# Kernel tuning notes

Hardware: AMD Instinct MI355X
Metric: run time of the kernel (lower is better)

Reference implementation:

```python
import jax, jax.numpy as jnp
import numpy as np

N, E, D_IN, HID, HEADS, TS_OUT = 100000, 200000, 165, 64, 8, 5
HD1 = HID // HEADS  # 8 per-head channels in layer 1
HD2 = HID           # 64 per-head channels in layer 2 (concat=False -> mean)


def _glorot(key, shape):
    fan_in, fan_out = shape[0], shape[1]
    s = np.sqrt(6.0 / (fan_in + fan_out)).astype(np.float32)
    return jax.random.uniform(key, shape, jnp.float32, -s, s)


def setup_inputs() -> dict:
    key = jax.random.key(0)
    ks = jax.random.split(key, 24)
    inp = {
        "x": jax.random.normal(ks[0], (N, D_IN), jnp.float32),
        "edge_index": jax.random.randint(ks[1], (2, E), 0, N, jnp.int32),
        "timestamp_target": jax.random.randint(ks[2], (N,), 0, TS_OUT, jnp.int32),
        "node_target": jax.random.randint(ks[3], (N,), 0, 2, jnp.int32),
        "node_mask": jax.random.randint(ks[4], (N,), 0, 2, jnp.int32).astype(jnp.bool_),
        # GATConv layer 1: in=165 -> 8 heads x 8 ch, concat -> 64
        "W1": _glorot(ks[5], (D_IN, HEADS * HD1)),
        "att_src1": _glorot(ks[6], (HEADS, HD1)),
        "att_dst1": _glorot(ks[7], (HEADS, HD1)),
        "b1": jnp.zeros((HEADS * HD1,), jnp.float32),
        # GATConv layer 2: in=64 -> 8 heads x 64 ch, mean -> 64
        "W2": _glorot(ks[8], (HID, HEADS * HD2)),
        "att_src2": _glorot(ks[9], (HEADS, HD2)),
        "att_dst2": _glorot(ks[10], (HEADS, HD2)),
        "b2": jnp.zeros((HD2,), jnp.float32),
        # timestamp predictor MLP
        "ts_w1": _glorot(ks[11], (HID, HID)), "ts_b1": jnp.zeros((HID,), jnp.float32),
        "ts_w2": _glorot(ks[12], (HID, TS_OUT)), "ts_b2": jnp.zeros((TS_OUT,), jnp.float32),
        # class predictor MLP
        "cls_w1": _glorot(ks[13], (HID, HID)), "cls_b1": jnp.zeros((HID,), jnp.float32),
        "cls_w2": _glorot(ks[14], (HID, 2)), "cls_b2": jnp.zeros((2,), jnp.float32),
    }
    return inp


def _gat_layer(x, src, dst, n, W, a_src, a_dst, b, concat):
    H, C = a_src.shape
    h = (x @ W).reshape(n, H, C)                      # [N,H,C]
    a_s = (h * a_src).sum(-1)                         # [N,H]
    a_d = (h * a_dst).sum(-1)                         # [N,H]
    alpha = jax.nn.leaky_relu(a_s[src] + a_d[dst], 0.2)   # [E,H]
    amax = jax.ops.segment_max(alpha, dst, num_segments=n)
    ea = jnp.exp(alpha - amax[dst])
    denom = jax.ops.segment_sum(ea, dst, num_segments=n)
    a = ea / (denom[dst] + 1e-16)                     # segment softmax over incoming edges
    out = jax.ops.segment_sum(h[src] * a[:, :, None], dst, num_segments=n)  # [N,H,C]
    out = out.reshape(n, H * C) if concat else out.mean(axis=1)
    return out + b


def _ce(logits, targets):
    lp = jax.nn.log_softmax(logits, axis=-1)
    return -jnp.take_along_axis(lp, targets[:, None].astype(jnp.int32), axis=1)[:, 0]


def reference(x, edge_index, timestamp_target, node_target, node_mask,
              W1, att_src1, att_dst1, b1, W2, att_src2, att_dst2, b2,
              ts_w1, ts_b1, ts_w2, ts_b2, cls_w1, cls_b1, cls_w2, cls_b2):
    n = x.shape[0]
    loops = jnp.arange(n, dtype=edge_index.dtype)
    src = jnp.concatenate([edge_index[0], loops])     # add self loops (PyG default)
    dst = jnp.concatenate([edge_index[1], loops])
    h = _gat_layer(x, src, dst, n, W1, att_src1, att_dst1, b1, True)   # [N,64]
    h = _gat_layer(h, src, dst, n, W2, att_src2, att_dst2, b2, False)  # [N,64]
    # gradient reversal is identity in the forward pass
    ts_pred = jax.nn.relu(h @ ts_w1 + ts_b1) @ ts_w2 + ts_b2           # [N,5]
    cls_pred = jax.nn.relu(h @ cls_w1 + cls_b1) @ cls_w2 + cls_b2      # [N,2]
    ts_loss = _ce(ts_pred, timestamp_target).mean()
    m = node_mask.astype(jnp.float32)
    cls_loss = (_ce(cls_pred, node_target) * m).sum() / m.sum()
    return cls_loss + 1.0 * ts_loss
```

## Files before the change

### kernel.cpp

```cpp
#include <hip/hip_runtime.h>
#include <hip/hip_bf16.h>

#define NN 100000
#define NE 200000
#define NT (NE + NN)
#define DIN 165
#define CHUNK 50000
#define PREPB 128
#define INITB 391
#define PACKB 8
#define W1PB 24
#define MISCGRID (PREPB + INITB + PACKB + W1PB)
#define NODEB 1563

typedef __attribute__((ext_vector_type(8))) short bf16x8_t;
typedef __attribute__((ext_vector_type(4))) float f32x4_t;
typedef _Float16 h2_t __attribute__((ext_vector_type(2)));
typedef _Float16 f16x8_t __attribute__((ext_vector_type(8)));

#define AS1 __attribute__((address_space(1)))
#define AS3 __attribute__((address_space(3)))

static __device__ __forceinline__ unsigned short f2bf(float f) {
    __hip_bfloat16 b = __float2bfloat16(f);
    return *(unsigned short*)&b;
}
static __device__ __forceinline__ float bfu(unsigned short u) {
    __hip_bfloat16 b = *(__hip_bfloat16*)&u;
    return __bfloat162float(b);
}
static __device__ __forceinline__ unsigned pkh2(float a, float b) {
    h2_t v; v[0] = (_Float16)a; v[1] = (_Float16)b;
    return *(unsigned*)&v;
}


__global__ __launch_bounds__(256) void k_misc(const float* W2, const float* a2s, const float* a2d,
                                              float* wsd, __hip_bfloat16* W2pT,
                                              int* cnt, int* fill,
                                              const float* tsw1, const float* cw1,
                                              unsigned* tswp, unsigned* cwp,
                                              const float* W1, unsigned* W1pT, float* zbuf) {
    int b = blockIdx.x;
    int tid = threadIdx.x;
    if (b < PREPB) {
        int i = b * 256 + tid;
        int c = i >> 9, j = i & 511;
        int hh = j >> 6, kk = j & 63;
        W2pT[i] = __float2bfloat16(W2[kk * 512 + hh * 64 + c]);
        if (b == 0 && tid < 64) zbuf[tid] = 0.f;
        if (i < 512) {
            int h = i >> 6, k = i & 63;
            float s = 0.f, d = 0.f;
            for (int cc = 0; cc < 64; cc++) {
                float w = W2[k * 512 + h * 64 + cc];
                s += w * a2s[h * 64 + cc];
                d += w * a2d[h * 64 + cc];
            }
            wsd[i] = s; wsd[512 + i] = d;
        }
    } else if (b < PREPB + INITB) {
        int i = (b - PREPB) * 256 + tid;
        if (i < NN) { cnt[i] = 0; fill[i] = 0; }
    } else if (b < PREPB + INITB + PACKB) {
        int i = (b - PREPB - INITB) * 256 + tid;
        if (i < 2048) {
            int kp = i >> 6, c = i & 63;
            tswp[i] = pkh2(tsw1[(2 * kp) * 64 + c], tsw1[(2 * kp + 1) * 64 + c]);
            cwp[i]  = pkh2(cw1[(2 * kp) * 64 + c],  cw1[(2 * kp + 1) * 64 + c]);
        }
    } else {
        int i = (b - PREPB - INITB - PACKB) * 256 + tid;
        if (i < 6144) {
            int c = i / 96, kp = i - c * 96;
            int k = 2 * kp;
            float f0 = (k < DIN) ? W1[k * 64 + c] : 0.f;
            float f1 = (k + 1 < DIN) ? W1[(k + 1) * 64 + c] : 0.f;
            W1pT[i] = pkh2(f0, f1);
        }
    }
}


__global__ __launch_bounds__(256) void k_count(const int* dstE, int* cnt) {
    int e = blockIdx.x * 256 + threadIdx.x;
    if (e < NE) atomicAdd(&cnt[dstE[e]], 1);
}

__global__ __launch_bounds__(256) void k_scanA(const int* cnt, int* rowptr, int* bsum) {
    __shared__ int sm[256];
    int t = threadIdx.x;
    int base = blockIdx.x * 1024;
    int v[4]; int s = 0;
    for (int i = 0; i < 4; i++) {
        int idx = base + t * 4 + i;
        v[i] = (idx < NN) ? (cnt[idx] + 1) : 0;
        s += v[i];
    }
    sm[t] = s; __syncthreads();
    for (int off = 1; off < 256; off <<= 1) {
        int x = (t >= off) ? sm[t - off] : 0;
        __syncthreads();
        sm[t] += x;
        __syncthreads();
    }
    int run = sm[t] - s;
    for (int i = 0; i < 4; i++) {
        run += v[i];
        int idx = base + t * 4 + i;
        if (idx < NN) rowptr[idx + 1] = run;
    }
    if (t == 255) bsum[blockIdx.x] = sm[255];
}

__global__ __launch_bounds__(64) void k_scanB(int* bsum, int nb) {
    int lane = threadIdx.x;
    int v0 = (lane < nb) ? bsum[lane] : 0;
    int v1 = (64 + lane < nb) ? bsum[64 + lane] : 0;
    int s0 = v0;
    for (int off = 1; off < 64; off <<= 1) { int t = __shfl_up(s0, off); if (lane >= off) s0 += t; }
    int tot0 = __shfl(s0, 63);
    int s1 = v1;
    for (int off = 1; off < 64; off <<= 1) { int t = __shfl_up(s1, off); if (lane >= off) s1 += t; }
    if (lane < nb) bsum[lane] = s0 - v0;
    if (64 + lane < nb) bsum[64 + lane] = tot0 + s1 - v1;
}

__global__ __launch_bounds__(256) void k_scanC(const int* bsum, int* rowptr) {
    int i = blockIdx.x * 256 + threadIdx.x;
    if (i < NN) rowptr[i + 1] += bsum[i >> 10];
    if (i == 0) rowptr[0] = 0;
}

__global__ __launch_bounds__(256) void k_fill(const int* srcE, const int* dstE,
                                              const int* rowptr, int* fill, int* col, int* rowv) {
    int i = blockIdx.x * 256 + threadIdx.x;
    if (i >= NT) return;
    int s, d;
    if (i < NE) { s = srcE[i]; d = dstE[i]; }
    else        { s = i - NE; d = s; }
    int p = rowptr[d] + atomicAdd(&fill[d], 1);
    col[p] = s;
    rowv[p] = d;
}


__global__ __launch_bounds__(256) void k_gemm1(const float* x, const unsigned* W1pT,
                                               const float* att_s, const float* att_d,
                                               const float* zsrc,
                                               __hip_bfloat16* h1b, float* aad1) {
    __shared__ float As[4][3 * 512];
    int tid = threadIdx.x;
    int l = tid & 63, w = tid >> 6;
    int n0 = blockIdx.x * 64 + w * 16;
    float* bufs = As[w];
    int frow = l & 15;
    int kg = l >> 4;
    int rl = l >> 5;
    int j2 = l & 3;
    int pb = (l >> 2) & 7;
    f32x4_t acc[4] = {};

#define G1_DMA(S, BI)                                                              \
    {                                                                              \
        float* dst_ = bufs + (BI) * 512;                                           \
        _Pragma("unroll")                                                          \
        for (int i_ = 0; i_ < 8; i_++) {                                           \
            int r_ = i_ * 2 + rl;                                                  \
            int kk_ = ((pb ^ (r_ & 7)) << 2) | j2;                                 \
            int k_ = (S) * 32 + kk_;                                               \
            int n_ = n0 + r_;                                                      \
            const float* g_ = (n_ < NN && k_ < DIN) ? (x + (size_t)n_ * DIN + k_)  \
                                                    : (zsrc + l);                  \
            __builtin_amdgcn_global_load_lds((const AS1 float*)g_,                 \
                                             (AS3 float*)(dst_ + i_ * 64), 4, 0, 0); \
        }                                                                          \
    }

#define G1_LB(DST, S)                                                              \
    _Pragma("unroll")                                                              \
    for (int t_ = 0; t_ < 4; t_++)                                                 \
        DST[t_] = *(const uint4*)&W1pT[(t_ * 16 + frow) * 96 + (S) * 16 + kg * 4];

#define G1_STEP(S, VM)                                                             \
    {                                                                              \
        __builtin_amdgcn_sched_barrier(0);                                         \
        if ((S) < 5) { G1_LB(Bn, (S) + 1) }                                        \
        __builtin_amdgcn_sched_barrier(0);                                         \
        if ((S) < 4) { G1_DMA((S) + 2, ((S) + 2) % 3) }                            \
        __builtin_amdgcn_sched_barrier(0);                                         \
        asm volatile("s_waitcnt vmcnt(" #VM ")" ::: "memory");                     \
        __builtin_amdgcn_sched_barrier(0);                                         \
        {                                                                          \
            float* cb_ = bufs + ((S) % 3) * 512;                                   \
            int b0_ = ((2 * kg) ^ (frow & 7)) * 4;                                 \
            int b1_ = ((2 * kg + 1) ^ (frow & 7)) * 4;                             \
            float4 f0 = *(const float4*)&cb_[frow * 32 + b0_];                     \
            float4 f1 = *(const float4*)&cb_[frow * 32 + b1_];                     \
            f16x8_t av;                                                            \
            av[0] = (_Float16)f0.x; av[1] = (_Float16)f0.y;                        \
            av[2] = (_Float16)f0.z; av[3] = (_Float16)f0.w;                        \
            av[4] = (_Float16)f1.x; av[5] = (_Float16)f1.y;                        \
            av[6] = (_Float16)f1.z; av[7] = (_Float16)f1.w;                        \
            _Pragma("unroll")                                                      \
            for (int t_ = 0; t_ < 4; t_++)                                         \
                acc[t_] = __builtin_amdgcn_mfma_f32_16x16x32_f16(                  \
                    av, *(f16x8_t*)&Bn0[t_], acc[t_], 0, 0, 0);                    \
            _Pragma("unroll")                                                      \
            for (int t_ = 0; t_ < 4; t_++) Bn0[t_] = Bn[t_];                       \
        }                                                                          \
    }

    uint4 Bn0[4], Bn[4];
    G1_DMA(0, 0)
    G1_DMA(1, 1)
    G1_LB(Bn0, 0)
    G1_STEP(0, 12)
    G1_STEP(1, 20)
    G1_STEP(2, 20)
    G1_STEP(3, 20)
    G1_STEP(4, 12)
    G1_STEP(5, 0)

    unsigned short* h1u = (unsigned short*)h1b;
    float asv[4], adv[4];
    #pragma unroll
    for (int t = 0; t < 4; t++) {
        int c = t * 16 + frow;
        asv[t] = att_s[c]; adv[t] = att_d[c];
    }
    int hb = (l >> 3) & 1;
    #pragma unroll
    for (int q = 0; q < 4; q++) {
        int n = n0 + kg * 4 + q;
        bool ok = (n < NN);
        #pragma unroll
        for (int t = 0; t < 4; t++) {
            if (ok) h1u[(size_t)n * 64 + t * 16 + frow] = f2bf(acc[t][q]);
            float sv = acc[t][q] * asv[t];
            float dv = acc[t][q] * adv[t];
            sv += __shfl_xor(sv, 1); sv += __shfl_xor(sv, 2); sv += __shfl_xor(sv, 4);
            dv += __shfl_xor(dv, 1); dv += __shfl_xor(dv, 2); dv += __shfl_xor(dv, 4);
            if (ok && (l & 7) == 0) {
                int h = t * 2 + hb;
                aad1[(size_t)n * 16 + h]     = sv;
                aad1[(size_t)n * 16 + 8 + h] = dv;
            }
        }
    }
}


__global__ __launch_bounds__(256) void k_edgew(const float* aad, const int* col, const int* rowv,
                                               __hip_bfloat16* web) {
    int e = blockIdx.x * 256 + threadIdx.x;
    if (e >= NT) return;
    int s = col[e], d = rowv[e];
    float4 s0 = *(const float4*)&aad[(size_t)s * 16];
    float4 s1 = *(const float4*)&aad[(size_t)s * 16 + 4];
    float4 dd0 = *(const float4*)&aad[(size_t)d * 16 + 8];
    float4 dd1 = *(const float4*)&aad[(size_t)d * 16 + 12];
    float as[8] = {s0.x, s0.y, s0.z, s0.w, s1.x, s1.y, s1.z, s1.w};
    float ad[8] = {dd0.x, dd0.y, dd0.z, dd0.w, dd1.x, dd1.y, dd1.z, dd1.w};
    unsigned p[4];
    #pragma unroll
    for (int q = 0; q < 4; q++) {
        float a0 = as[2*q]   + ad[2*q];
        float a1 = as[2*q+1] + ad[2*q+1];
        a0 = a0 > 0.f ? a0 : 0.2f * a0;
        a1 = a1 > 0.f ? a1 : 0.2f * a1;
        p[q] = (unsigned)f2bf(__expf(a0)) | ((unsigned)f2bf(__expf(a1)) << 16);
    }
    *(uint4*)&web[(size_t)e * 8] = make_uint4(p[0], p[1], p[2], p[3]);
}


__global__ __launch_bounds__(256) void k_agg1(const __hip_bfloat16* h1b, const __hip_bfloat16* we1b,
                                              const int* rowptr, const int* col,
                                              const float* b1, __hip_bfloat16* out1b) {
    int tid = threadIdx.x;
    int q = tid & 15;
    int n = blockIdx.x * 16 + (tid >> 4);
    int hq = q >> 1;
    const unsigned short* h1u = (const unsigned short*)h1b;
    const unsigned short* weu = (const unsigned short*)we1b;
    int rs = rowptr[n], re = rowptr[n + 1];
    float acc0 = 0.f, acc1 = 0.f, acc2 = 0.f, acc3 = 0.f, den = 0.f;
    for (int eb = rs; eb < re; eb += 4) {
        int c4[4];
        #pragma unroll
        for (int j = 0; j < 4; j++) c4[j] = col[min(eb + j, re - 1)];
        #pragma unroll
        for (int j = 0; j < 4; j++) {
            int e = min(eb + j, re - 1);
            float wv = bfu(weu[(size_t)e * 8 + hq]);
            wv = (eb + j < re) ? wv : 0.f;
            uint2 hv = *(const uint2*)&h1u[(size_t)c4[j] * 64 + q * 4];
            den  += wv;
            acc0 += wv * bfu((unsigned short)(hv.x & 0xffff));
            acc1 += wv * bfu((unsigned short)(hv.x >> 16));
            acc2 += wv * bfu((unsigned short)(hv.y & 0xffff));
            acc3 += wv * bfu((unsigned short)(hv.y >> 16));
        }
    }
    float4 bb = *(const float4*)&b1[q * 4];
    float dd = den + 1e-16f;
    unsigned short* ou = (unsigned short*)out1b;
    unsigned p0 = (unsigned)f2bf(acc0 / dd + bb.x) | ((unsigned)f2bf(acc1 / dd + bb.y) << 16);
    unsigned p1 = (unsigned)f2bf(acc2 / dd + bb.z) | ((unsigned)f2bf(acc3 / dd + bb.w) << 16);
    *(uint2*)&ou[(size_t)n * 64 + q * 4] = make_uint2(p0, p1);
}


__global__ __launch_bounds__(256) void k_att2(const __hip_bfloat16* out1b, const float* wsd,
                                              float* aad2) {
    __shared__ float t[64][65];
    int tid = threadIdx.x;
    int n0 = blockIdx.x * 64;
    const unsigned short* o1u = (const unsigned short*)out1b;
    #pragma unroll
    for (int l = 0; l < 4; l++) {
        int q = tid + l * 256;
        int r = q >> 4, c4 = q & 15;
        int n = n0 + r;
        uint2 v = make_uint2(0, 0);
        if (n < NN) v = *(const uint2*)&o1u[(size_t)n * 64 + c4 * 4];
        t[r][c4 * 4 + 0] = bfu((unsigned short)(v.x & 0xffff));
        t[r][c4 * 4 + 1] = bfu((unsigned short)(v.x >> 16));
        t[r][c4 * 4 + 2] = bfu((unsigned short)(v.y & 0xffff));
        t[r][c4 * 4 + 3] = bfu((unsigned short)(v.y >> 16));
    }
    __syncthreads();
    int lane = tid & 63;
    int j0 = __builtin_amdgcn_readfirstlane((tid >> 6) * 4);
    int n = n0 + lane;
    float a0 = 0.f, a1 = 0.f, a2 = 0.f, a3 = 0.f;
    #pragma unroll 8
    for (int k = 0; k < 64; k++) {
        float ov = t[lane][k];
        a0 += ov * wsd[(j0 + 0) * 64 + k];
        a1 += ov * wsd[(j0 + 1) * 64 + k];
        a2 += ov * wsd[(j0 + 2) * 64 + k];
        a3 += ov * wsd[(j0 + 3) * 64 + k];
    }
    if (n < NN) *(float4*)&aad2[(size_t)n * 16 + j0] = make_float4(a0, a1, a2, a3);
}


__global__ __launch_bounds__(256) void k_agg2(const __hip_bfloat16* out1b, const __hip_bfloat16* we2b,
                                              const int* rowptr, const int* col,
                                              __hip_bfloat16* aggb, int n0, int n1) {
    int tid = threadIdx.x;
    int p = tid & 31;
    int n = n0 + blockIdx.x * 8 + (tid >> 5);
    const unsigned short* o1u = (const unsigned short*)out1b;
    const unsigned short* weu = (const unsigned short*)we2b;
    int rs = rowptr[n], re = rowptr[n + 1];
    float den[8] = {}, a0[8] = {}, a1[8] = {};
    for (int eb = rs; eb < re; eb += 4) {
        int c4[4];
        #pragma unroll
        for (int j = 0; j < 4; j++) c4[j] = col[min(eb + j, re - 1)];
        #pragma unroll
        for (int j = 0; j < 4; j++) {
            int e = min(eb + j, re - 1);
            uint4 wv = *(const uint4*)&weu[(size_t)e * 8];
            unsigned hv = *(const unsigned*)&o1u[(size_t)c4[j] * 64 + p * 2];
            float vmul = (eb + j < re) ? 1.f : 0.f;
            float h0 = bfu((unsigned short)(hv & 0xffff));
            float h1 = bfu((unsigned short)(hv >> 16));
            float wts[8] = {bfu((unsigned short)(wv.x & 0xffff)), bfu((unsigned short)(wv.x >> 16)),
                            bfu((unsigned short)(wv.y & 0xffff)), bfu((unsigned short)(wv.y >> 16)),
                            bfu((unsigned short)(wv.z & 0xffff)), bfu((unsigned short)(wv.z >> 16)),
                            bfu((unsigned short)(wv.w & 0xffff)), bfu((unsigned short)(wv.w >> 16))};
            #pragma unroll
            for (int hh = 0; hh < 8; hh++) {
                float ww = wts[hh] * vmul;
                den[hh] += ww;
                a0[hh] += ww * h0;
                a1[hh] += ww * h1;
            }
        }
    }
    size_t base = (size_t)(n - n0) * 512;
    unsigned short* au = (unsigned short*)aggb;
    #pragma unroll
    for (int hh = 0; hh < 8; hh++) {
        float dd = den[hh] + 1e-16f;
        unsigned pp = (unsigned)f2bf(a0[hh] / dd) | ((unsigned)f2bf(a1[hh] / dd) << 16);
        *(unsigned*)&au[base + hh * 64 + p * 2] = pp;
    }
}


__global__ __launch_bounds__(256) void k_gemm2(const __hip_bfloat16* aggb, const __hip_bfloat16* W2pT,
                                               const float* b2, __hip_bfloat16* out2Tb, int n0, int n1) {
    __shared__ float smem[4608];
    unsigned short* A_lds = (unsigned short*)smem;
    unsigned short* B_lds = A_lds + 64 * 72;
    const unsigned short* A_g = (const unsigned short*)aggb;
    const unsigned short* B_g = (const unsigned short*)W2pT;
    int tid = threadIdx.x;
    int w = tid >> 6, l = tid & 63;
    int m0 = blockIdx.x * 64;
    int rows = n1 - n0;
    f32x4_t acc[4] = {};
    for (int k0 = 0; k0 < 512; k0 += 64) {
        #pragma unroll
        for (int ll = 0; ll < 2; ll++) {
            int u = tid + ll * 256;
            int r = u >> 3, seg = u & 7;
            uint4 va = make_uint4(0, 0, 0, 0);
            if (m0 + r < rows) va = *(const uint4*)&A_g[(size_t)(m0 + r) * 512 + k0 + seg * 8];
            *(uint4*)&A_lds[r * 72 + seg * 8] = va;
            *(uint4*)&B_lds[r * 72 + seg * 8] = *(const uint4*)&B_g[(size_t)r * 512 + k0 + seg * 8];
        }
        __syncthreads();
        #pragma unroll
        for (int kk = 0; kk < 2; kk++) {
            bf16x8_t a = *(const bf16x8_t*)&A_lds[(w * 16 + (l & 15)) * 72 + kk * 32 + (l >> 4) * 8];
            #pragma unroll
            for (int t = 0; t < 4; t++) {
                bf16x8_t bb = *(const bf16x8_t*)&B_lds[(t * 16 + (l & 15)) * 72 + kk * 32 + (l >> 4) * 8];
                acc[t] = __builtin_amdgcn_mfma_f32_16x16x32_bf16(a, bb, acc[t], 0, 0, 0);
            }
        }
        __syncthreads();
    }
    #pragma unroll
    for (int t = 0; t < 4; t++) {
        int col_l = l & 15;
        float bias = b2[t * 16 + col_l];
        #pragma unroll
        for (int q = 0; q < 4; q++) {
            int row_l = (l >> 4) * 4 + q;
            smem[(w * 16 + row_l) * 66 + t * 16 + col_l] = 0.125f * acc[t][q] + bias;
        }
    }
    __syncthreads();
    unsigned short* o2u = (unsigned short*)out2Tb;
    int ml = tid & 63, cr = tid >> 6;
    #pragma unroll
    for (int p = 0; p < 16; p++) {
        int c = p * 4 + cr;
        int gr = m0 + ml;
        if (gr < rows) o2u[(size_t)c * NN + (n0 + gr)] = f2bf(smem[ml * 66 + c]);
    }
}


__global__ __launch_bounds__(256) void k_mlp(const __hip_bfloat16* out2Tb,
                                             const unsigned* tswp, const float* tsb1,
                                             const float* tsw2, const float* tsb2,
                                             const unsigned* cwp, const float* cb1,
                                             const float* cw2, const float* cb2,
                                             const int* tst, const int* ctg, const unsigned char* msk,
                                             float* part) {
    __shared__ unsigned t2h[32 * 64];
    __shared__ float red[4][7][64];
    int tid = threadIdx.x;
    int lane = tid & 63;
    int w = tid >> 6;
    int n0 = blockIdx.x * 64;
    int nstage = n0 + lane; if (nstage >= NN) nstage = NN - 1;
    const unsigned short* o2u = (const unsigned short*)out2Tb;
    #pragma unroll
    for (int l = 0; l < 8; l++) {
        int kp = w * 8 + l;
        float e0 = bfu(o2u[(size_t)(2 * kp) * NN + nstage]);
        float e1 = bfu(o2u[(size_t)(2 * kp + 1) * NN + nstage]);
        t2h[kp * 64 + lane] = pkh2(e0, e1);
    }
    __syncthreads();

    int c0 = __builtin_amdgcn_readfirstlane(w * 16);
    int n = n0 + lane;
    float vts[16], vcls[16];
    #pragma unroll
    for (int j = 0; j < 16; j++) { vts[j] = tsb1[c0 + j]; vcls[j] = cb1[c0 + j]; }
    for (int kp = 0; kp < 32; kp++) {
        unsigned ou = t2h[kp * 64 + lane];
        h2_t ov = *(h2_t*)&ou;
        const unsigned* wt = &tswp[kp * 64 + c0];
        const unsigned* wc = &cwp[kp * 64 + c0];
        #pragma unroll
        for (int j = 0; j < 16; j++) {
            unsigned wtv = wt[j], wcv = wc[j];
            vts[j]  = __builtin_amdgcn_fdot2(ov, *(h2_t*)&wtv, vts[j], false);
            vcls[j] = __builtin_amdgcn_fdot2(ov, *(h2_t*)&wcv, vcls[j], false);
        }
    }
    float lg[5] = {0.f, 0.f, 0.f, 0.f, 0.f};
    float lg2[2] = {0.f, 0.f};
    #pragma unroll
    for (int j = 0; j < 16; j++) {
        int c = c0 + j;
        float v = fmaxf(vts[j], 0.f);
        #pragma unroll
        for (int t = 0; t < 5; t++) lg[t] += v * tsw2[c * 5 + t];
        float v2 = fmaxf(vcls[j], 0.f);
        lg2[0] += v2 * cw2[c * 2];
        lg2[1] += v2 * cw2[c * 2 + 1];
    }
    #pragma unroll
    for (int t = 0; t < 5; t++) red[w][t][lane] = lg[t];
    red[w][5][lane] = lg2[0];
    red[w][6][lane] = lg2[1];
    __syncthreads();
    if (w == 0) {
        float tsl = 0.f, cll = 0.f, mval = 0.f;
        if (n < NN) {
            float L[5];
            #pragma unroll
            for (int t = 0; t < 5; t++)
                L[t] = red[0][t][lane] + red[1][t][lane] + red[2][t][lane] + red[3][t][lane] + tsb2[t];
            float mx = L[0];
            #pragma unroll
            for (int t = 1; t < 5; t++) mx = fmaxf(mx, L[t]);
            float se = 0.f;
            #pragma unroll
            for (int t = 0; t < 5; t++) se += __expf(L[t] - mx);
            int tg = tst[n];
            float pick = 0.f;
            #pragma unroll
            for (int t = 0; t < 5; t++) pick += (t == tg) ? L[t] : 0.f;
            tsl = mx + __logf(se) - pick;
            float C0 = red[0][5][lane] + red[1][5][lane] + red[2][5][lane] + red[3][5][lane] + cb2[0];
            float C1 = red[0][6][lane] + red[1][6][lane] + red[2][6][lane] + red[3][6][lane] + cb2[1];
            float mx2 = fmaxf(C0, C1);
            float lse2 = mx2 + __logf(__expf(C0 - mx2) + __expf(C1 - mx2));
            mval = msk[n] ? 1.f : 0.f;
            float pick2 = ctg[n] ? C1 : C0;
            cll = (lse2 - pick2) * mval;
        }
        #pragma unroll
        for (int off = 1; off < 64; off <<= 1) {
            tsl  += __shfl_xor(tsl, off);
            cll  += __shfl_xor(cll, off);
            mval += __shfl_xor(mval, off);
        }
        if (lane == 0) {
            part[blockIdx.x * 3 + 0] = tsl;
            part[blockIdx.x * 3 + 1] = cll;
            part[blockIdx.x * 3 + 2] = mval;
        }
    }
}

__global__ __launch_bounds__(256) void k_final(const float* part, float* out, int nb) {
    __shared__ float sm[3][256];
    int tid = threadIdx.x;
    float a = 0, b = 0, c = 0;
    for (int i = tid; i < nb; i += 256) { a += part[i*3]; b += part[i*3+1]; c += part[i*3+2]; }
    sm[0][tid] = a; sm[1][tid] = b; sm[2][tid] = c;
    __syncthreads();
    for (int s = 128; s > 0; s >>= 1) {
        if (tid < s) {
            sm[0][tid] += sm[0][tid + s];
            sm[1][tid] += sm[1][tid + s];
            sm[2][tid] += sm[2][tid + s];
        }
        __syncthreads();
    }
    if (tid == 0) out[0] = sm[1][0] / sm[2][0] + sm[0][0] / (float)NN;
}


extern "C" void kernel_launch(void* const* d_in, const int* in_sizes, int n_in,
                              void* d_out, int out_size, void* d_ws, size_t ws_size,
                              hipStream_t stream) {
    const float* x    = (const float*)d_in[0];
    const int*   ei   = (const int*)d_in[1];
    const int*   tst  = (const int*)d_in[2];
    const int*   ctg  = (const int*)d_in[3];
    const unsigned char* msk = (const unsigned char*)d_in[4];
    const float* W1   = (const float*)d_in[5];
    const float* a1s  = (const float*)d_in[6];
    const float* a1d  = (const float*)d_in[7];
    const float* b1   = (const float*)d_in[8];
    const float* W2   = (const float*)d_in[9];
    const float* a2s  = (const float*)d_in[10];
    const float* a2d  = (const float*)d_in[11];
    const float* b2   = (const float*)d_in[12];
    const float* tsw1 = (const float*)d_in[13];
    const float* tsb1 = (const float*)d_in[14];
    const float* tsw2 = (const float*)d_in[15];
    const float* tsb2 = (const float*)d_in[16];
    const float* cw1  = (const float*)d_in[17];
    const float* cb1  = (const float*)d_in[18];
    const float* cw2  = (const float*)d_in[19];
    const float* cb2  = (const float*)d_in[20];
    const int* srcE = ei;
    const int* dstE = ei + NE;

    char* ws = (char*)d_ws;
    size_t off = 0;
    auto alloc = [&](size_t b) { size_t o = off; off = (off + b + 255) & ~(size_t)255; return o; };
    int*   cnt    = (int*)(ws + alloc((size_t)NN * 4));
    int*   fill   = (int*)(ws + alloc((size_t)NN * 4));
    int*   rowptr = (int*)(ws + alloc((size_t)(NN + 1) * 4));
    int*   bsum   = (int*)(ws + alloc(128 * 4));
    int*   col    = (int*)(ws + alloc((size_t)NT * 4));
    int*   rowv   = (int*)(ws + alloc((size_t)NT * 4));
    float* aad1   = (float*)(ws + alloc((size_t)NN * 16 * 4));
    __hip_bfloat16* out1b = (__hip_bfloat16*)(ws + alloc((size_t)NN * 64 * 2));
    float* aad2   = (float*)(ws + alloc((size_t)NN * 16 * 4));
    float* wsd    = (float*)(ws + alloc(1024 * 4));
    __hip_bfloat16* W2pT  = (__hip_bfloat16*)(ws + alloc(32768 * 2));
    unsigned* tswp = (unsigned*)(ws + alloc(2048 * 4));
    unsigned* cwp  = (unsigned*)(ws + alloc(2048 * 4));
    unsigned* W1pT = (unsigned*)(ws + alloc(6144 * 4));
    float* zbuf   = (float*)(ws + alloc(64 * 4));
    __hip_bfloat16* out2Tb = (__hip_bfloat16*)(ws + alloc((size_t)NN * 64 * 2));
    __hip_bfloat16* h1b   = (__hip_bfloat16*)(ws + alloc((size_t)NN * 64 * 2));
    __hip_bfloat16* aggb  = (__hip_bfloat16*)(ws + alloc((size_t)CHUNK * 512 * 2));
    __hip_bfloat16* web   = (__hip_bfloat16*)(ws + alloc((size_t)NT * 8 * 2));
    float* part   = (float*)(ws + alloc((size_t)NODEB * 3 * 4));
    (void)ws_size; (void)in_sizes; (void)n_in; (void)out_size;

    int nb_scan = (NN + 1023) / 1024;

    k_misc<<<MISCGRID, 256, 0, stream>>>(W2, a2s, a2d, wsd, W2pT, cnt, fill,
                                         tsw1, cw1, tswp, cwp, W1, W1pT, zbuf);
    k_count<<<(NE + 255) / 256, 256, 0, stream>>>(dstE, cnt);
    k_scanA<<<nb_scan, 256, 0, stream>>>(cnt, rowptr, bsum);
    k_scanB<<<1, 64, 0, stream>>>(bsum, nb_scan);
    k_scanC<<<(NN + 255) / 256, 256, 0, stream>>>(bsum, rowptr);
    k_fill<<<(NT + 255) / 256, 256, 0, stream>>>(srcE, dstE, rowptr, fill, col, rowv);

    k_gemm1<<<NODEB, 256, 0, stream>>>(x, W1pT, a1s, a1d, zbuf, h1b, aad1);
    k_edgew<<<(NT + 255) / 256, 256, 0, stream>>>(aad1, col, rowv, web);
    k_agg1<<<NN / 16, 256, 0, stream>>>(h1b, web, rowptr, col, b1, out1b);
    k_att2<<<NODEB, 256, 0, stream>>>(out1b, wsd, aad2);
    k_edgew<<<(NT + 255) / 256, 256, 0, stream>>>(aad2, col, rowv, web);

    for (int c = 0; c < 2; c++) {
        int n0 = c * CHUNK, n1 = n0 + CHUNK;
        k_agg2<<<CHUNK / 8, 256, 0, stream>>>(out1b, web, rowptr, col, aggb, n0, n1);
        k_gemm2<<<(CHUNK + 63) / 64, 256, 0, stream>>>(aggb, W2pT, b2, out2Tb, n0, n1);
    }

    k_mlp<<<NODEB, 256, 0, stream>>>(out2Tb, tswp, tsb1, tsw2, tsb2,
                                     cwp, cb1, cw2, cb2, tst, ctg, msk, part);
    k_final<<<1, 256, 0, stream>>>(part, (float*)d_out, NODEB);
}
```

Measured before the change: 214.2 us.

## Load whole x tile with wide LDS DMA and stage h1 stores through LDS

```diff
diff --git a/kernel.cpp b/kernel.cpp
--- a/kernel.cpp
+++ b/kernel.cpp
@@ -12,6 +12,8 @@
 #define W1PB 24
 #define MISCGRID (PREPB + INITB + PACKB + W1PB)
 #define NODEB 1563
+#define XDW ((size_t)NN * DIN)
+#define NDMA 42
 
 typedef __attribute__((ext_vector_type(8))) short bf16x8_t;
 typedef __attribute__((ext_vector_type(4))) float f32x4_t;
@@ -48,7 +50,7 @@
         int c = i >> 9, j = i & 511;
         int hh = j >> 6, kk = j & 63;
         W2pT[i] = __float2bfloat16(W2[kk * 512 + hh * 64 + c]);
-        if (b == 0 && tid < 64) zbuf[tid] = 0.f;
+        if (b == 0) zbuf[tid] = 0.f;
         if (i < 512) {
             int h = i >> 6, k = i & 63;
             float s = 0.f, d = 0.f;
@@ -149,80 +151,43 @@
                                                const float* att_s, const float* att_d,
                                                const float* zsrc,
                                                __hip_bfloat16* h1b, float* aad1) {
-    __shared__ float As[4][3 * 512];
+    __shared__ float X[NDMA * 256];
     int tid = threadIdx.x;
     int l = tid & 63, w = tid >> 6;
-    int n0 = blockIdx.x * 64 + w * 16;
-    float* bufs = As[w];
-    int frow = l & 15;
-    int kg = l >> 4;
-    int rl = l >> 5;
-    int j2 = l & 3;
-    int pb = (l >> 2) & 7;
+    int n0 = blockIdx.x * 64;
+    int frow = l & 15, kg = l >> 4;
+
+    size_t tb = (size_t)n0 * DIN;
+    for (int i = w; i < NDMA; i += 4) {
+        size_t gd = tb + (size_t)i * 256 + (size_t)l * 4;
+        const float* g = (gd + 4 <= XDW) ? (x + gd) : (zsrc + l * 4);
+        __builtin_amdgcn_global_load_lds((const AS1 float*)g,
+                                         (AS3 float*)(X + i * 256), 16, 0, 0);
+    }
+    uint4 B[6][4];
+    #pragma unroll
+    for (int s = 0; s < 6; s++)
+        #pragma unroll
+        for (int t = 0; t < 4; t++)
+            B[s][t] = *(const uint4*)&W1pT[(t * 16 + frow) * 96 + s * 16 + kg * 4];
+    __syncthreads();
+
     f32x4_t acc[4] = {};
-
-#define G1_DMA(S, BI)                                                              \
-    {                                                                              \
-        float* dst_ = bufs + (BI) * 512;                                           \
-        _Pragma("unroll")                                                          \
-        for (int i_ = 0; i_ < 8; i_++) {                                           \
-            int r_ = i_ * 2 + rl;                                                  \
-            int kk_ = ((pb ^ (r_ & 7)) << 2) | j2;                                 \
-            int k_ = (S) * 32 + kk_;                                               \
-            int n_ = n0 + r_;                                                      \
-            const float* g_ = (n_ < NN && k_ < DIN) ? (x + (size_t)n_ * DIN + k_)  \
-                                                    : (zsrc + l);                  \
-            __builtin_amdgcn_global_load_lds((const AS1 float*)g_,                 \
-                                             (AS3 float*)(dst_ + i_ * 64), 4, 0, 0); \
-        }                                                                          \
-    }
-
-#define G1_LB(DST, S)                                                              \
-    _Pragma("unroll")                                                              \
-    for (int t_ = 0; t_ < 4; t_++)                                                 \
-        DST[t_] = *(const uint4*)&W1pT[(t_ * 16 + frow) * 96 + (S) * 16 + kg * 4];
-
-#define G1_STEP(S, VM)                                                             \
-    {                                                                              \
-        __builtin_amdgcn_sched_barrier(0);                                         \
-        if ((S) < 5) { G1_LB(Bn, (S) + 1) }                                        \
-        __builtin_amdgcn_sched_barrier(0);                                         \
-        if ((S) < 4) { G1_DMA((S) + 2, ((S) + 2) % 3) }                            \
-        __builtin_amdgcn_sched_barrier(0);                                         \
-        asm volatile("s_waitcnt vmcnt(" #VM ")" ::: "memory");                     \
-        __builtin_amdgcn_sched_barrier(0);                                         \
-        {                                                                          \
-            float* cb_ = bufs + ((S) % 3) * 512;                                   \
-            int b0_ = ((2 * kg) ^ (frow & 7)) * 4;                                 \
-            int b1_ = ((2 * kg + 1) ^ (frow & 7)) * 4;                             \
-            float4 f0 = *(const float4*)&cb_[frow * 32 + b0_];                     \
-            float4 f1 = *(const float4*)&cb_[frow * 32 + b1_];                     \
-            f16x8_t av;                                                            \
-            av[0] = (_Float16)f0.x; av[1] = (_Float16)f0.y;                        \
-            av[2] = (_Float16)f0.z; av[3] = (_Float16)f0.w;                        \
-            av[4] = (_Float16)f1.x; av[5] = (_Float16)f1.y;                        \
-            av[6] = (_Float16)f1.z; av[7] = (_Float16)f1.w;                        \
-            _Pragma("unroll")                                                      \
-            for (int t_ = 0; t_ < 4; t_++)                                         \
-                acc[t_] = __builtin_amdgcn_mfma_f32_16x16x32_f16(                  \
-                    av, *(f16x8_t*)&Bn0[t_], acc[t_], 0, 0, 0);                    \
-            _Pragma("unroll")                                                      \
-            for (int t_ = 0; t_ < 4; t_++) Bn0[t_] = Bn[t_];                       \
-        }                                                                          \
-    }
-
-    uint4 Bn0[4], Bn[4];
-    G1_DMA(0, 0)
-    G1_DMA(1, 1)
-    G1_LB(Bn0, 0)
-    G1_STEP(0, 12)
-    G1_STEP(1, 20)
-    G1_STEP(2, 20)
-    G1_STEP(3, 20)
-    G1_STEP(4, 12)
-    G1_STEP(5, 0)
-
-    unsigned short* h1u = (unsigned short*)h1b;
+    int rbase = (w * 16 + frow) * DIN + kg * 8;
+    #pragma unroll
+    for (int s = 0; s < 6; s++) {
+        float f[8];
+        #pragma unroll
+        for (int j = 0; j < 8; j++) f[j] = X[rbase + s * 32 + j];
+        f16x8_t av;
+        #pragma unroll
+        for (int j = 0; j < 8; j++) av[j] = (_Float16)f[j];
+        #pragma unroll
+        for (int t = 0; t < 4; t++)
+            acc[t] = __builtin_amdgcn_mfma_f32_16x16x32_f16(av, *(f16x8_t*)&B[s][t], acc[t], 0, 0, 0);
+    }
+
+    int nw = n0 + w * 16;
     float asv[4], adv[4];
     #pragma unroll
     for (int t = 0; t < 4; t++) {
@@ -232,11 +197,10 @@
     int hb = (l >> 3) & 1;
     #pragma unroll
     for (int q = 0; q < 4; q++) {
-        int n = n0 + kg * 4 + q;
+        int n = nw + kg * 4 + q;
         bool ok = (n < NN);
         #pragma unroll
         for (int t = 0; t < 4; t++) {
-            if (ok) h1u[(size_t)n * 64 + t * 16 + frow] = f2bf(acc[t][q]);
             float sv = acc[t][q] * asv[t];
             float dv = acc[t][q] * adv[t];
             sv += __shfl_xor(sv, 1); sv += __shfl_xor(sv, 2); sv += __shfl_xor(sv, 4);
@@ -247,6 +211,21 @@
                 aad1[(size_t)n * 16 + 8 + h] = dv;
             }
         }
+    }
+
+    __syncthreads();
+    unsigned short* Hw = (unsigned short*)X + w * 1152;
+    #pragma unroll
+    for (int t = 0; t < 4; t++)
+        #pragma unroll
+        for (int q = 0; q < 4; q++)
+            Hw[(kg * 4 + q) * 72 + t * 16 + frow] = f2bf(acc[t][q]);
+    int rr = l >> 2, cc = l & 3;
+    int n2 = nw + rr;
+    if (n2 < NN) {
+        unsigned short* dst = (unsigned short*)h1b + (size_t)n2 * 64 + cc * 16;
+        *(uint4*)dst       = *(const uint4*)&Hw[rr * 72 + cc * 16];
+        *(uint4*)(dst + 8) = *(const uint4*)&Hw[rr * 72 + cc * 16 + 8];
     }
 }
 
@@ -610,7 +589,7 @@
     unsigned* tswp = (unsigned*)(ws + alloc(2048 * 4));
     unsigned* cwp  = (unsigned*)(ws + alloc(2048 * 4));
     unsigned* W1pT = (unsigned*)(ws + alloc(6144 * 4));
-    float* zbuf   = (float*)(ws + alloc(64 * 4));
+    float* zbuf   = (float*)(ws + alloc(256 * 4));
     __hip_bfloat16* out2Tb = (__hip_bfloat16*)(ws + alloc((size_t)NN * 64 * 2));
     __hip_bfloat16* h1b   = (__hip_bfloat16*)(ws + alloc((size_t)NN * 64 * 2));
     __hip_bfloat16* aggb  = (__hip_bfloat16*)(ws + alloc((size_t)CHUNK * 512 * 2));
```

New measurement: 213.5 us. No clear change (-0.3%).
